# Kernel tuning notes

Measured on AMD Instinct MI355X. Metric: run time of the kernel, lower is better.

The kernel has to match this reference:

```python
import jax, jax.numpy as jnp
import numpy as np
import math

B, S, D, H = 2, 2048, 1024, 16
DH = D // H  # head_dim = 64


def setup_inputs() -> dict:
    key = jax.random.key(0)
    k0, k1, k2 = jax.random.split(key, 3)
    x = jax.random.normal(k0, (B, S, D), dtype=jnp.float32)
    Wi = jax.random.normal(k1, (3 * D, D), dtype=jnp.float32) * 0.02  # torch (out,in) layout
    bi = jnp.zeros((3 * D,), dtype=jnp.float32)
    Wo = jax.random.normal(k2, (D, D), dtype=jnp.float32) * 0.02
    bo = jnp.zeros((D,), dtype=jnp.float32)
    return {"x": x, "Wi": Wi, "bi": bi, "Wo": Wo, "bo": bo, "causal_mask": 1}


def reference(x, Wi, bi, Wo, bo, causal_mask):
    b, s, d = x.shape
    # fused QKV projection: nn.Linear applies x @ W.T + b
    qkv = x @ Wi.T + bi                      # (b, s, 3d)
    q, k, v = jnp.split(qkv, 3, axis=-1)
    # (b, s, d) -> (b, h, s, dh)
    def to_heads(t):
        return t.reshape(b, s, H, DH).transpose(0, 2, 1, 3)
    q, k, v = to_heads(q), to_heads(k), to_heads(v)
    scores = jnp.einsum("bhqd,bhkd->bhqk", q, k)  # (b, h, s, s)
    if causal_mask:
        # mask strictly-upper triangle with -inf BEFORE scaling (as in source; -inf unaffected)
        tri = jnp.triu(jnp.ones((s, s), dtype=bool), k=1)
        scores = jnp.where(tri, -jnp.inf, scores)
    scores = scores / math.sqrt(DH)
    weight = jax.nn.softmax(scores, axis=-1)
    out = jnp.einsum("bhqk,bhkd->bhqd", weight, v)  # (b, h, s, dh)
    out = out.transpose(0, 2, 1, 3).reshape(b, s, d)
    return out @ Wo.T + bo
```

## Files before the change

### kernel.cpp

```cpp
#include <hip/hip_runtime.h>
#include <hip/hip_bf16.h>
#include <stdint.h>

#define B_    2
#define S_    2048
#define D_    1024
#define H_    16
#define DH_   64
#define MTOT  (B_*S_)
#define NQKV  (3*D_)

typedef __attribute__((ext_vector_type(8))) short  bf16x8;
typedef __attribute__((ext_vector_type(4))) short  bf16x4;
typedef __attribute__((ext_vector_type(4))) float  f32x4;
typedef __attribute__((ext_vector_type(8))) unsigned short u16x8;
typedef unsigned short ushort_t;

__device__ __forceinline__ ushort_t f2bf(float f) {
  union { float f; unsigned int i; } v; v.f = f;
  unsigned int r = v.i + 0x7FFF + ((v.i >> 16) & 1);
  return (ushort_t)(r >> 16);
}

__device__ __forceinline__ unsigned cvt_pk_bf16(float lo, float hi) {
  unsigned r;
  asm("v_cvt_pk_bf16_f32 %0, %1, %2" : "=v"(r) : "v"(lo), "v"(hi));
  return r;
}

__device__ __forceinline__ float fexp2(float x) {
  float r;
  asm("v_exp_f32 %0, %1" : "=v"(r) : "v"(x));
  return r;
}

#if __has_builtin(__builtin_amdgcn_mfma_f32_16x16x16_bf16)
__device__ __forceinline__ f32x4 mfma16(bf16x4 a, bf16x4 b, f32x4 c) {
  return __builtin_amdgcn_mfma_f32_16x16x16_bf16(a, b, c, 0, 0, 0);
}
#elif __has_builtin(__builtin_amdgcn_mfma_f32_16x16x16bf16_1k)
__device__ __forceinline__ f32x4 mfma16(bf16x4 a, bf16x4 b, f32x4 c) {
  return __builtin_amdgcn_mfma_f32_16x16x16bf16_1k(a, b, c, 0, 0, 0);
}
#else
__device__ __forceinline__ f32x4 mfma16(bf16x4 a, bf16x4 b, f32x4 c) {
  asm volatile("v_mfma_f32_16x16x16_bf16 %0, %1, %2, %0"
               : "+v"(c) : "v"(a), "v"(b));
  return c;
}
#endif

__device__ __forceinline__ void gl_lds16(const ushort_t* g, ushort_t* l) {
  __builtin_amdgcn_global_load_lds(
      (const __attribute__((address_space(1))) unsigned int*)g,
      (__attribute__((address_space(3))) unsigned int*)l, 16, 0, 0);
}

#define CVN1 (MTOT*D_/8)
#define CVN2 (NQKV*D_/8)
#define CVN3 (D_*D_/8)
__global__ __launch_bounds__(256) void cvt_all(
    const float* __restrict__ x, const float* __restrict__ Wi, const float* __restrict__ Wo,
    ushort_t* __restrict__ xb, ushort_t* __restrict__ Wib, ushort_t* __restrict__ Wob) {
  int i = blockIdx.x * blockDim.x + threadIdx.x;
  const float* src; ushort_t* dst; int k;
  if (i < CVN1)            { src = x;  dst = xb;  k = i; }
  else if (i < CVN1+CVN2)  { src = Wi; dst = Wib; k = i - CVN1; }
  else                     { src = Wo; dst = Wob; k = i - CVN1 - CVN2; }
  const float4* s4 = (const float4*)src;
  float4 a = s4[2*k], b = s4[2*k+1];
  u16x8 o;
  o[0]=f2bf(a.x); o[1]=f2bf(a.y); o[2]=f2bf(a.z); o[3]=f2bf(a.w);
  o[4]=f2bf(b.x); o[5]=f2bf(b.y); o[6]=f2bf(b.z); o[7]=f2bf(b.w);
  ((u16x8*)dst)[k] = o;
}

#define BKg 32
#define QSCALE 0.18033688011112042f
__global__ __launch_bounds__(256) void gemm_qkv(
    const ushort_t* __restrict__ Abf, const ushort_t* __restrict__ Bbf,
    const float* __restrict__ bias,
    ushort_t* __restrict__ qb, ushort_t* __restrict__ kb, ushort_t* __restrict__ vb) {
  __shared__ __align__(16) ushort_t Al[128*BKg];
  __shared__ __align__(16) ushort_t Bl[128*BKg];
  int tid = threadIdx.x;
  int w = tid >> 6, lane = tid & 63;
  int wrow = (w >> 1) * 64, wcol = (w & 1) * 64;
  int m0 = blockIdx.y * 128, n0 = blockIdx.x * 128;
  const int K = D_;
  f32x4 zero = {0.f, 0.f, 0.f, 0.f};
  f32x4 acc[4][4];
  for (int i=0;i<4;i++) for (int j=0;j<4;j++) acc[i][j] = zero;

  for (int k0 = 0; k0 < K; k0 += BKg) {
    __syncthreads();
    for (int it = 0; it < 2; ++it) {
      int c = it*256 + tid;
      int row = c >> 2, cc = c & 3;
      int lbase = (it*256 + w*64) * 8;
      gl_lds16(Abf + (size_t)(m0+row)*K + k0 + cc*8, Al + lbase);
      gl_lds16(Bbf + (size_t)(n0+row)*K + k0 + cc*8, Bl + lbase);
    }
    asm volatile("s_waitcnt vmcnt(0)" ::: "memory");
    __syncthreads();
    int kof = (lane >> 4) * 8;
    bf16x8 af[4], bfr[4];
    for (int i=0;i<4;i++) af[i]  = *(const bf16x8*)(Al + (wrow + i*16 + (lane&15))*BKg + kof);
    for (int j=0;j<4;j++) bfr[j] = *(const bf16x8*)(Bl + (wcol + j*16 + (lane&15))*BKg + kof);
    for (int i=0;i<4;i++)
      for (int j=0;j<4;j++)
        acc[i][j] = __builtin_amdgcn_mfma_f32_16x16x32_bf16(af[i], bfr[j], acc[i][j], 0, 0, 0);
  }
  for (int i=0;i<4;i++)
    for (int j=0;j<4;j++)
      for (int r=0;r<4;r++) {
        int gm = m0 + wrow + i*16 + (lane>>4)*4 + r;
        int gn = n0 + wcol + j*16 + (lane&15);
        float v = acc[i][j][r] + bias[gn];
        int b = gm >> 11, s = gm & (S_-1);
        int sect = gn >> 10, hn = gn & (D_-1);
        int hh = hn >> 6, d = hn & 63;
        size_t idx = (((size_t)(b*H_ + hh))*S_ + s)*DH_ + d;
        if (sect == 0) v *= QSCALE;
        ushort_t val = f2bf(v);
        if (sect == 0) qb[idx] = val;
        else if (sect == 1) kb[idx] = val;
        else vb[idx] = val;
      }
}

__global__ __launch_bounds__(256) void transpose_v(
    const ushort_t* __restrict__ vb, ushort_t* __restrict__ vtb) {
  __shared__ ushort_t T[64*72];
  int bh = blockIdx.y;
  int s0 = blockIdx.x * 64;
  int tid = threadIdx.x;
  const ushort_t* src = vb + (size_t)bh * S_ * DH_;
  ushort_t* dst = vtb + (size_t)bh * DH_ * S_;
  for (int it = 0; it < 2; ++it) {
    int c = it*256 + tid;
    int row = c >> 3, cc = c & 7;
    *(uint4*)&T[row*72 + cc*8] = *(const uint4*)(src + (size_t)(s0+row)*DH_ + cc*8);
  }
  __syncthreads();
  for (int it = 0; it < 2; ++it) {
    int c = it*256 + tid;
    int d = c >> 3, sc = c & 7;
    u16x8 o;
    #pragma unroll
    for (int e = 0; e < 8; ++e) o[e] = T[(sc*8+e)*72 + d];
    *(u16x8*)(dst + (size_t)d*S_ + s0 + sc*8) = o;
  }
}

#define KVB 64
#define DTHR 8.0f
__global__ __launch_bounds__(512) void attn_fwd(
    const ushort_t* __restrict__ qb, const ushort_t* __restrict__ kb,
    const ushort_t* __restrict__ vtb, ushort_t* __restrict__ attnb,
    const int* __restrict__ causal) {
  int wg = blockIdx.x;
  int xcd = wg & 7;
  int rest = wg >> 3;
  int bh = (rest & 3) * 8 + xcd;
  int qblk = 15 - (rest >> 2);
  int b = bh >> 4, h = bh & 15;
  int tid = threadIdx.x, w = tid >> 6, lane = tid & 63;
  int g = lane >> 4, q16 = lane & 15;
  const ushort_t* qh  = qb  + (size_t)bh * S_ * DH_;
  const ushort_t* kh  = kb  + (size_t)bh * S_ * DH_;
  const ushort_t* vth = vtb + (size_t)bh * DH_ * S_;
  __shared__ __align__(16) ushort_t Kl[3][KVB*64];
  __shared__ __align__(16) ushort_t Vtl[3][64*KVB];
  bool use_causal = (causal[0] != 0);

  int nkv = use_causal ? (2*qblk + 2) : (S_/KVB);
  int qw = qblk*128 + w*16;

  bf16x8 qc0 = *(const bf16x8*)(qh + (size_t)(qw + q16)*DH_ +  0 + g*8);
  bf16x8 qc1 = *(const bf16x8*)(qh + (size_t)(qw + q16)*DH_ + 32 + g*8);

  int r0 = tid >> 3, sw0 = ((tid & 7) ^ (r0 & 7)) * 8;
  const ushort_t* kp0 = kh  + (size_t)r0 * DH_ + sw0;
  const ushort_t* vp0 = vth + (size_t)r0 * S_  + sw0;

  auto stage = [&](int t, int buf) {
    gl_lds16(kp0 + (size_t)(t*KVB) * DH_, &Kl[buf][tid*8]);
    gl_lds16(vp0 + t*KVB,                 &Vtl[buf][tid*8]);
  };

  f32x4 zero = {0.f,0.f,0.f,0.f};
  f32x4 o[4];
  #pragma unroll
  for (int dt=0;dt<4;dt++) o[dt] = zero;
  float mrun = -1e30f, lrun = 0.f;

  stage(0, 0);
  stage(1, 1);
  asm volatile("s_waitcnt vmcnt(2)" ::: "memory");
  __builtin_amdgcn_s_barrier();

  for (int it = 0; it < nkv; ++it) {
    int cur = it % 3;
    int kvbase = it * KVB;
    if (it + 2 < nkv) stage(it + 2, (it + 2) % 3);

    f32x4 sacc[4];
    #pragma unroll
    for (int j=0;j<4;j++) sacc[j] = zero;
    #pragma unroll
    for (int kk=0;kk<2;kk++) {
      bf16x8 qf = kk ? qc1 : qc0;
      #pragma unroll
      for (int j=0;j<4;j++) {
        int row = j*16 + q16;
        int slot = (kk*4 + g) ^ (row & 7);
        bf16x8 kf = *(const bf16x8*)(&Kl[cur][row*64 + slot*8]);
        sacc[j] = __builtin_amdgcn_mfma_f32_16x16x32_bf16(kf, qf, sacc[j], 0, 0, 0);
      }
    }
    if (use_causal && kvbase + KVB - 1 > qw) {
      int qd = qw + q16 - kvbase;
      #pragma unroll
      for (int j=0;j<4;j++)
        #pragma unroll
        for (int r=0;r<4;r++)
          if (16*j + 4*g + r > qd) sacc[j][r] = -1e30f;
    }
    float m0v = fmaxf(fmaxf(sacc[0][0], sacc[0][1]), fmaxf(sacc[0][2], sacc[0][3]));
    float m1v = fmaxf(fmaxf(sacc[1][0], sacc[1][1]), fmaxf(sacc[1][2], sacc[1][3]));
    float m2v = fmaxf(fmaxf(sacc[2][0], sacc[2][1]), fmaxf(sacc[2][2], sacc[2][3]));
    float m3v = fmaxf(fmaxf(sacc[3][0], sacc[3][1]), fmaxf(sacc[3][2], sacc[3][3]));
    float mx = fmaxf(fmaxf(m0v, m1v), fmaxf(m2v, m3v));
    mx = fmaxf(mx, __shfl_xor(mx, 16, 64));
    mx = fmaxf(mx, __shfl_xor(mx, 32, 64));
    if (!__all(mx - mrun <= DTHR)) {
      float mnew = fmaxf(mrun, mx);
      float alpha = fexp2(mrun - mnew);
      lrun *= alpha;
      float av0 = __shfl(alpha, 4*g + 0, 64);
      float av1 = __shfl(alpha, 4*g + 1, 64);
      float av2 = __shfl(alpha, 4*g + 2, 64);
      float av3 = __shfl(alpha, 4*g + 3, 64);
      #pragma unroll
      for (int dt=0;dt<4;dt++) {
        o[dt][0] *= av0; o[dt][1] *= av1; o[dt][2] *= av2; o[dt][3] *= av3;
      }
      mrun = mnew;
    }
    float p[4][4];
    float rs = 0.f;
    #pragma unroll
    for (int j=0;j<4;j++)
      #pragma unroll
      for (int r=0;r<4;r++) {
        p[j][r] = fexp2(sacc[j][r] - mrun);
        rs += p[j][r];
      }
    rs += __shfl_xor(rs, 16, 64);
    rs += __shfl_xor(rs, 32, 64);
    lrun += rs;
    #pragma unroll
    for (int s=0;s<4;s++) {
      union { unsigned u[2]; bf16x4 v; } pk;
      pk.u[0] = cvt_pk_bf16(p[s][0], p[s][1]);
      pk.u[1] = cvt_pk_bf16(p[s][2], p[s][3]);
      int E = 16*s + 4*g;
      #pragma unroll
      for (int dt=0;dt<4;dt++) {
        int row = dt*16 + q16;
        int off = row*64 + ((E >> 3) ^ (row & 7))*8 + (E & 7);
        bf16x4 vf = *(const bf16x4*)(&Vtl[cur][off]);
        o[dt] = mfma16(pk.v, vf, o[dt]);
      }
    }
    if (it + 2 < nkv) {
      asm volatile("s_waitcnt vmcnt(2)" ::: "memory");
    } else {
      asm volatile("s_waitcnt vmcnt(0)" ::: "memory");
    }
    __builtin_amdgcn_s_barrier();
  }
  float li0 = 1.f / __shfl(lrun, 4*g + 0, 64);
  float li1 = 1.f / __shfl(lrun, 4*g + 1, 64);
  float li2 = 1.f / __shfl(lrun, 4*g + 2, 64);
  float li3 = 1.f / __shfl(lrun, 4*g + 3, 64);
  #pragma unroll
  for (int r=0;r<4;r++) {
    float li = (r==0)?li0:(r==1)?li1:(r==2)?li2:li3;
    int q = qw + 4*g + r;
    #pragma unroll
    for (int dt=0;dt<4;dt++) {
      int d = dt*16 + q16;
      attnb[((size_t)(b*S_ + q))*D_ + h*DH_ + d] = f2bf(o[dt][r] * li);
    }
  }
}

__global__ __launch_bounds__(256) void gemm_out(
    const ushort_t* __restrict__ Abf, const ushort_t* __restrict__ Bbf,
    const float* __restrict__ bias, float* __restrict__ out) {
  __shared__ __align__(16) ushort_t Al[128*BKg];
  __shared__ __align__(16) ushort_t Bl[128*BKg];
  int tid = threadIdx.x;
  int w = tid >> 6, lane = tid & 63;
  int wrow = (w >> 1) * 64, wcol = (w & 1) * 64;
  int m0 = blockIdx.y * 128, n0 = blockIdx.x * 128;
  const int K = D_;
  f32x4 zero = {0.f,0.f,0.f,0.f};
  f32x4 acc[4][4];
  for (int i=0;i<4;i++) for (int j=0;j<4;j++) acc[i][j] = zero;

  for (int k0 = 0; k0 < K; k0 += BKg) {
    __syncthreads();
    for (int it = 0; it < 2; ++it) {
      int c = it*256 + tid;
      int row = c >> 2, cc = c & 3;
      int lbase = (it*256 + w*64) * 8;
      gl_lds16(Abf + (size_t)(m0+row)*K + k0 + cc*8, Al + lbase);
      gl_lds16(Bbf + (size_t)(n0+row)*K + k0 + cc*8, Bl + lbase);
    }
    asm volatile("s_waitcnt vmcnt(0)" ::: "memory");
    __syncthreads();
    int kof = (lane >> 4) * 8;
    bf16x8 af[4], bfr[4];
    for (int i=0;i<4;i++) af[i]  = *(const bf16x8*)(Al + (wrow + i*16 + (lane&15))*BKg + kof);
    for (int j=0;j<4;j++) bfr[j] = *(const bf16x8*)(Bl + (wcol + j*16 + (lane&15))*BKg + kof);
    for (int i=0;i<4;i++)
      for (int j=0;j<4;j++)
        acc[i][j] = __builtin_amdgcn_mfma_f32_16x16x32_bf16(af[i], bfr[j], acc[i][j], 0, 0, 0);
  }
  for (int i=0;i<4;i++)
    for (int j=0;j<4;j++)
      for (int r=0;r<4;r++) {
        int gm = m0 + wrow + i*16 + (lane>>4)*4 + r;
        int gn = n0 + wcol + j*16 + (lane&15);
        out[(size_t)gm*D_ + gn] = acc[i][j][r] + bias[gn];
      }
}

extern "C" void kernel_launch(void* const* d_in, const int* in_sizes, int n_in,
                              void* d_out, int out_size, void* d_ws, size_t ws_size,
                              hipStream_t stream) {
  const float* x  = (const float*)d_in[0];
  const float* Wi = (const float*)d_in[1];
  const float* bi = (const float*)d_in[2];
  const float* Wo = (const float*)d_in[3];
  const float* bo = (const float*)d_in[4];
  const int* causal = (const int*)d_in[5];
  float* out = (float*)d_out;

  ushort_t* xb   = (ushort_t*)d_ws;
  ushort_t* Wib  = xb  + (size_t)MTOT*D_;
  ushort_t* Wob  = Wib + (size_t)NQKV*D_;
  ushort_t* qbuf = Wob + (size_t)D_*D_;
  ushort_t* kbuf = qbuf + (size_t)B_*H_*S_*DH_;
  ushort_t* vbuf = kbuf + (size_t)B_*H_*S_*DH_;
  ushort_t* attnb = vbuf + (size_t)B_*H_*S_*DH_;
  ushort_t* vtb  = xb;

  int ntot = CVN1 + CVN2 + CVN3;
  cvt_all<<<(ntot+255)/256, 256, 0, stream>>>(x, Wi, Wo, xb, Wib, Wob);

  gemm_qkv<<<dim3(NQKV/128, MTOT/128), 256, 0, stream>>>(xb, Wib, bi, qbuf, kbuf, vbuf);
  transpose_v<<<dim3(S_/64, B_*H_), 256, 0, stream>>>(vbuf, vtb);
  attn_fwd<<<512, 512, 0, stream>>>(qbuf, kbuf, vtb, attnb, causal);
  gemm_out<<<dim3(D_/128, MTOT/128), 256, 0, stream>>>(attnb, Wob, bo, out);
}
```

Before: 123.3 us.

## Double-buffer GEMM LDS tiles and halve attention query block size

Both the QKV and output GEMMs now keep two LDS buffers. The next K-tile is prefetched while MFMAs run on the current one, which is meant to hide global-load latency that was previously serialized behind a full wait. The attention kernel moves from 128-query, 512-thread blocks to 64-query, 256-thread blocks, doubling the grid to 1024 workgroups for finer causal load balancing. Each thread now stages two K/V chunks. The cost is double the GEMM LDS footprint, plus more K/V reloads in attention because each block covers fewer queries.

```diff
diff --git a/kernel.cpp b/kernel.cpp
--- a/kernel.cpp
+++ b/kernel.cpp
@@ -81,35 +81,45 @@
     const ushort_t* __restrict__ Abf, const ushort_t* __restrict__ Bbf,
     const float* __restrict__ bias,
     ushort_t* __restrict__ qb, ushort_t* __restrict__ kb, ushort_t* __restrict__ vb) {
-  __shared__ __align__(16) ushort_t Al[128*BKg];
-  __shared__ __align__(16) ushort_t Bl[128*BKg];
+  __shared__ __align__(16) ushort_t Al[2][128*BKg];
+  __shared__ __align__(16) ushort_t Bl[2][128*BKg];
   int tid = threadIdx.x;
   int w = tid >> 6, lane = tid & 63;
   int wrow = (w >> 1) * 64, wcol = (w & 1) * 64;
   int m0 = blockIdx.y * 128, n0 = blockIdx.x * 128;
   const int K = D_;
-  f32x4 zero = {0.f, 0.f, 0.f, 0.f};
-  f32x4 acc[4][4];
-  for (int i=0;i<4;i++) for (int j=0;j<4;j++) acc[i][j] = zero;
-
-  for (int k0 = 0; k0 < K; k0 += BKg) {
-    __syncthreads();
+  const int nt = K / BKg;
+
+  auto stageg = [&](int t, int buf) {
+    int k0 = t * BKg;
+    #pragma unroll
     for (int it = 0; it < 2; ++it) {
       int c = it*256 + tid;
       int row = c >> 2, cc = c & 3;
       int lbase = (it*256 + w*64) * 8;
-      gl_lds16(Abf + (size_t)(m0+row)*K + k0 + cc*8, Al + lbase);
-      gl_lds16(Bbf + (size_t)(n0+row)*K + k0 + cc*8, Bl + lbase);
-    }
-    asm volatile("s_waitcnt vmcnt(0)" ::: "memory");
-    __syncthreads();
+      gl_lds16(Abf + (size_t)(m0+row)*K + k0 + cc*8, &Al[buf][lbase]);
+      gl_lds16(Bbf + (size_t)(n0+row)*K + k0 + cc*8, &Bl[buf][lbase]);
+    }
+  };
+
+  f32x4 zero = {0.f, 0.f, 0.f, 0.f};
+  f32x4 acc[4][4];
+  for (int i=0;i<4;i++) for (int j=0;j<4;j++) acc[i][j] = zero;
+
+  stageg(0, 0);
+  __syncthreads();
+
+  for (int t = 0; t < nt; ++t) {
+    int cur = t & 1;
+    if (t + 1 < nt) stageg(t + 1, cur ^ 1);
     int kof = (lane >> 4) * 8;
     bf16x8 af[4], bfr[4];
-    for (int i=0;i<4;i++) af[i]  = *(const bf16x8*)(Al + (wrow + i*16 + (lane&15))*BKg + kof);
-    for (int j=0;j<4;j++) bfr[j] = *(const bf16x8*)(Bl + (wcol + j*16 + (lane&15))*BKg + kof);
+    for (int i=0;i<4;i++) af[i]  = *(const bf16x8*)(&Al[cur][(wrow + i*16 + (lane&15))*BKg + kof]);
+    for (int j=0;j<4;j++) bfr[j] = *(const bf16x8*)(&Bl[cur][(wcol + j*16 + (lane&15))*BKg + kof]);
     for (int i=0;i<4;i++)
       for (int j=0;j<4;j++)
         acc[i][j] = __builtin_amdgcn_mfma_f32_16x16x32_bf16(af[i], bfr[j], acc[i][j], 0, 0, 0);
+    __syncthreads();
   }
   for (int i=0;i<4;i++)
     for (int j=0;j<4;j++)
@@ -155,7 +165,7 @@
 
 #define KVB 64
 #define DTHR 8.0f
-__global__ __launch_bounds__(512) void attn_fwd(
+__global__ __launch_bounds__(256) void attn_fwd(
     const ushort_t* __restrict__ qb, const ushort_t* __restrict__ kb,
     const ushort_t* __restrict__ vtb, ushort_t* __restrict__ attnb,
     const int* __restrict__ causal) {
@@ -163,7 +173,7 @@
   int xcd = wg & 7;
   int rest = wg >> 3;
   int bh = (rest & 3) * 8 + xcd;
-  int qblk = 15 - (rest >> 2);
+  int qblk = 31 - (rest >> 2);
   int b = bh >> 4, h = bh & 15;
   int tid = threadIdx.x, w = tid >> 6, lane = tid & 63;
   int g = lane >> 4, q16 = lane & 15;
@@ -174,19 +184,27 @@
   __shared__ __align__(16) ushort_t Vtl[3][64*KVB];
   bool use_causal = (causal[0] != 0);
 
-  int nkv = use_causal ? (2*qblk + 2) : (S_/KVB);
-  int qw = qblk*128 + w*16;
+  int nkv = use_causal ? (qblk + 1) : (S_/KVB);
+  int qw = qblk*64 + w*16;
 
   bf16x8 qc0 = *(const bf16x8*)(qh + (size_t)(qw + q16)*DH_ +  0 + g*8);
   bf16x8 qc1 = *(const bf16x8*)(qh + (size_t)(qw + q16)*DH_ + 32 + g*8);
 
-  int r0 = tid >> 3, sw0 = ((tid & 7) ^ (r0 & 7)) * 8;
-  const ushort_t* kp0 = kh  + (size_t)r0 * DH_ + sw0;
-  const ushort_t* vp0 = vth + (size_t)r0 * S_  + sw0;
+  int c0 = tid, c1 = tid + 256;
+  int r0 = c0 >> 3, sw0 = ((c0 & 7) ^ (r0 & 7)) * 8;
+  int r1 = c1 >> 3, sw1 = ((c1 & 7) ^ (r1 & 7)) * 8;
+  const ushort_t* kp0 = kh + r0*DH_ + sw0;
+  const ushort_t* kp1 = kh + r1*DH_ + sw1;
+  const ushort_t* vp0 = vth + (size_t)r0*S_ + sw0;
+  const ushort_t* vp1 = vth + (size_t)r1*S_ + sw1;
 
   auto stage = [&](int t, int buf) {
-    gl_lds16(kp0 + (size_t)(t*KVB) * DH_, &Kl[buf][tid*8]);
-    gl_lds16(vp0 + t*KVB,                 &Vtl[buf][tid*8]);
+    size_t kadv = (size_t)(t*KVB) * DH_;
+    int vadv = t*KVB;
+    gl_lds16(kp0 + kadv, &Kl[buf][c0*8]);
+    gl_lds16(kp1 + kadv, &Kl[buf][c1*8]);
+    gl_lds16(vp0 + vadv, &Vtl[buf][c0*8]);
+    gl_lds16(vp1 + vadv, &Vtl[buf][c1*8]);
   };
 
   f32x4 zero = {0.f,0.f,0.f,0.f};
@@ -197,7 +215,7 @@
 
   stage(0, 0);
   stage(1, 1);
-  asm volatile("s_waitcnt vmcnt(2)" ::: "memory");
+  asm volatile("s_waitcnt vmcnt(4)" ::: "memory");
   __builtin_amdgcn_s_barrier();
 
   for (int it = 0; it < nkv; ++it) {
@@ -275,7 +293,7 @@
       }
     }
     if (it + 2 < nkv) {
-      asm volatile("s_waitcnt vmcnt(2)" ::: "memory");
+      asm volatile("s_waitcnt vmcnt(4)" ::: "memory");
     } else {
       asm volatile("s_waitcnt vmcnt(0)" ::: "memory");
     }
@@ -300,35 +318,45 @@
 __global__ __launch_bounds__(256) void gemm_out(
     const ushort_t* __restrict__ Abf, const ushort_t* __restrict__ Bbf,
     const float* __restrict__ bias, float* __restrict__ out) {
-  __shared__ __align__(16) ushort_t Al[128*BKg];
-  __shared__ __align__(16) ushort_t Bl[128*BKg];
+  __shared__ __align__(16) ushort_t Al[2][128*BKg];
+  __shared__ __align__(16) ushort_t Bl[2][128*BKg];
   int tid = threadIdx.x;
   int w = tid >> 6, lane = tid & 63;
   int wrow = (w >> 1) * 64, wcol = (w & 1) * 64;
   int m0 = blockIdx.y * 128, n0 = blockIdx.x * 128;
   const int K = D_;
-  f32x4 zero = {0.f,0.f,0.f,0.f};
-  f32x4 acc[4][4];
-  for (int i=0;i<4;i++) for (int j=0;j<4;j++) acc[i][j] = zero;
-
-  for (int k0 = 0; k0 < K; k0 += BKg) {
-    __syncthreads();
+  const int nt = K / BKg;
+
+  auto stageg = [&](int t, int buf) {
+    int k0 = t * BKg;
+    #pragma unroll
     for (int it = 0; it < 2; ++it) {
       int c = it*256 + tid;
       int row = c >> 2, cc = c & 3;
       int lbase = (it*256 + w*64) * 8;
-      gl_lds16(Abf + (size_t)(m0+row)*K + k0 + cc*8, Al + lbase);
-      gl_lds16(Bbf + (size_t)(n0+row)*K + k0 + cc*8, Bl + lbase);
-    }
-    asm volatile("s_waitcnt vmcnt(0)" ::: "memory");
-    __syncthreads();
+      gl_lds16(Abf + (size_t)(m0+row)*K + k0 + cc*8, &Al[buf][lbase]);
+      gl_lds16(Bbf + (size_t)(n0+row)*K + k0 + cc*8, &Bl[buf][lbase]);
+    }
+  };
+
+  f32x4 zero = {0.f,0.f,0.f,0.f};
+  f32x4 acc[4][4];
+  for (int i=0;i<4;i++) for (int j=0;j<4;j++) acc[i][j] = zero;
+
+  stageg(0, 0);
+  __syncthreads();
+
+  for (int t = 0; t < nt; ++t) {
+    int cur = t & 1;
+    if (t + 1 < nt) stageg(t + 1, cur ^ 1);
     int kof = (lane >> 4) * 8;
     bf16x8 af[4], bfr[4];
-    for (int i=0;i<4;i++) af[i]  = *(const bf16x8*)(Al + (wrow + i*16 + (lane&15))*BKg + kof);
-    for (int j=0;j<4;j++) bfr[j] = *(const bf16x8*)(Bl + (wcol + j*16 + (lane&15))*BKg + kof);
+    for (int i=0;i<4;i++) af[i]  = *(const bf16x8*)(&Al[cur][(wrow + i*16 + (lane&15))*BKg + kof]);
+    for (int j=0;j<4;j++) bfr[j] = *(const bf16x8*)(&Bl[cur][(wcol + j*16 + (lane&15))*BKg + kof]);
     for (int i=0;i<4;i++)
       for (int j=0;j<4;j++)
         acc[i][j] = __builtin_amdgcn_mfma_f32_16x16x32_bf16(af[i], bfr[j], acc[i][j], 0, 0, 0);
+    __syncthreads();
   }
   for (int i=0;i<4;i++)
     for (int j=0;j<4;j++)
@@ -364,6 +392,6 @@
 
   gemm_qkv<<<dim3(NQKV/128, MTOT/128), 256, 0, stream>>>(xb, Wib, bi, qbuf, kbuf, vbuf);
   transpose_v<<<dim3(S_/64, B_*H_), 256, 0, stream>>>(vbuf, vtb);
-  attn_fwd<<<512, 512, 0, stream>>>(qbuf, kbuf, vtb, attnb, causal);
+  attn_fwd<<<1024, 256, 0, stream>>>(qbuf, kbuf, vtb, attnb, causal);
   gemm_out<<<dim3(D_/128, MTOT/128), 256, 0, stream>>>(attnb, Wob, bo, out);
 }
```

Measured after the change: 130.9 us. 1.06x slower.

## Use persistent attention blocks with per-XCD atomic work queues and smaller query tiles

Applied to the files above, without the earlier changes.

Turns attention into a persistent kernel of 768 blocks of 256 threads. Each block pulls work items from eight per-XCD atomic counters, longest causal rows first, and can steal from other queues once its own is empty. Query tiles shrink from 128 to 64 rows, and the counters are reset inside the conversion kernel. The goal is better load balance across the triangular causal workload; the cost is atomics, extra barriers and less K/V reuse per staged tile.

```diff
diff --git a/kernel.cpp b/kernel.cpp
--- a/kernel.cpp
+++ b/kernel.cpp
@@ -61,8 +61,10 @@
 #define CVN3 (D_*D_/8)
 __global__ __launch_bounds__(256) void cvt_all(
     const float* __restrict__ x, const float* __restrict__ Wi, const float* __restrict__ Wo,
-    ushort_t* __restrict__ xb, ushort_t* __restrict__ Wib, ushort_t* __restrict__ Wob) {
+    ushort_t* __restrict__ xb, ushort_t* __restrict__ Wib, ushort_t* __restrict__ Wob,
+    int* __restrict__ ctr) {
   int i = blockIdx.x * blockDim.x + threadIdx.x;
+  if (i < 8) ctr[i] = 0;
   const float* src; ushort_t* dst; int k;
   if (i < CVN1)            { src = x;  dst = xb;  k = i; }
   else if (i < CVN1+CVN2)  { src = Wi; dst = Wib; k = i - CVN1; }
@@ -155,144 +157,162 @@
 
 #define KVB 64
 #define DTHR 8.0f
-__global__ __launch_bounds__(512) void attn_fwd(
+__global__ __launch_bounds__(256) void attn_fwd(
     const ushort_t* __restrict__ qb, const ushort_t* __restrict__ kb,
     const ushort_t* __restrict__ vtb, ushort_t* __restrict__ attnb,
-    const int* __restrict__ causal) {
-  int wg = blockIdx.x;
-  int xcd = wg & 7;
-  int rest = wg >> 3;
-  int bh = (rest & 3) * 8 + xcd;
-  int qblk = 15 - (rest >> 2);
-  int b = bh >> 4, h = bh & 15;
+    const int* __restrict__ causal, int* __restrict__ ctr) {
   int tid = threadIdx.x, w = tid >> 6, lane = tid & 63;
   int g = lane >> 4, q16 = lane & 15;
-  const ushort_t* qh  = qb  + (size_t)bh * S_ * DH_;
-  const ushort_t* kh  = kb  + (size_t)bh * S_ * DH_;
-  const ushort_t* vth = vtb + (size_t)bh * DH_ * S_;
   __shared__ __align__(16) ushort_t Kl[3][KVB*64];
   __shared__ __align__(16) ushort_t Vtl[3][64*KVB];
+  __shared__ int e_sh;
   bool use_causal = (causal[0] != 0);
-
-  int nkv = use_causal ? (2*qblk + 2) : (S_/KVB);
-  int qw = qblk*128 + w*16;
-
-  bf16x8 qc0 = *(const bf16x8*)(qh + (size_t)(qw + q16)*DH_ +  0 + g*8);
-  bf16x8 qc1 = *(const bf16x8*)(qh + (size_t)(qw + q16)*DH_ + 32 + g*8);
-
-  int r0 = tid >> 3, sw0 = ((tid & 7) ^ (r0 & 7)) * 8;
-  const ushort_t* kp0 = kh  + (size_t)r0 * DH_ + sw0;
-  const ushort_t* vp0 = vth + (size_t)r0 * S_  + sw0;
-
-  auto stage = [&](int t, int buf) {
-    gl_lds16(kp0 + (size_t)(t*KVB) * DH_, &Kl[buf][tid*8]);
-    gl_lds16(vp0 + t*KVB,                 &Vtl[buf][tid*8]);
-  };
+  int myq = blockIdx.x & 7;
 
   f32x4 zero = {0.f,0.f,0.f,0.f};
-  f32x4 o[4];
-  #pragma unroll
-  for (int dt=0;dt<4;dt++) o[dt] = zero;
-  float mrun = -1e30f, lrun = 0.f;
-
-  stage(0, 0);
-  stage(1, 1);
-  asm volatile("s_waitcnt vmcnt(2)" ::: "memory");
-  __builtin_amdgcn_s_barrier();
-
-  for (int it = 0; it < nkv; ++it) {
-    int cur = it % 3;
-    int kvbase = it * KVB;
-    if (it + 2 < nkv) stage(it + 2, (it + 2) % 3);
-
-    f32x4 sacc[4];
-    #pragma unroll
-    for (int j=0;j<4;j++) sacc[j] = zero;
-    #pragma unroll
-    for (int kk=0;kk<2;kk++) {
-      bf16x8 qf = kk ? qc1 : qc0;
+
+  for (int qi = 0; qi < 8; ++qi) {
+    int qq = (myq + qi) & 7;
+    while (true) {
+      if (tid == 0) e_sh = atomicAdd(&ctr[qq], 1);
+      __syncthreads();
+      int e = e_sh;
+      if (e >= 128) break;
+      int qblk = 31 - (e >> 2);
+      int bh = qq + 8 * (e & 3);
+      int b = bh >> 4, h = bh & 15;
+      const ushort_t* qh  = qb  + (size_t)bh * S_ * DH_;
+      const ushort_t* kh  = kb  + (size_t)bh * S_ * DH_;
+      const ushort_t* vth = vtb + (size_t)bh * DH_ * S_;
+
+      int nkv = use_causal ? (qblk + 1) : (S_/KVB);
+      int qw = qblk*64 + w*16;
+
+      bf16x8 qc0 = *(const bf16x8*)(qh + (size_t)(qw + q16)*DH_ +  0 + g*8);
+      bf16x8 qc1 = *(const bf16x8*)(qh + (size_t)(qw + q16)*DH_ + 32 + g*8);
+
+      int c0 = tid, c1 = tid + 256;
+      int r0 = c0 >> 3, sw0 = ((c0 & 7) ^ (r0 & 7)) * 8;
+      int r1 = c1 >> 3, sw1 = ((c1 & 7) ^ (r1 & 7)) * 8;
+      const ushort_t* kp0 = kh + r0*DH_ + sw0;
+      const ushort_t* kp1 = kh + r1*DH_ + sw1;
+      const ushort_t* vp0 = vth + (size_t)r0*S_ + sw0;
+      const ushort_t* vp1 = vth + (size_t)r1*S_ + sw1;
+
+      auto stage = [&](int t, int buf) {
+        size_t kadv = (size_t)(t*KVB) * DH_;
+        int vadv = t*KVB;
+        gl_lds16(kp0 + kadv, &Kl[buf][c0*8]);
+        gl_lds16(kp1 + kadv, &Kl[buf][c1*8]);
+        gl_lds16(vp0 + vadv, &Vtl[buf][c0*8]);
+        gl_lds16(vp1 + vadv, &Vtl[buf][c1*8]);
+      };
+
+      f32x4 o[4];
       #pragma unroll
-      for (int j=0;j<4;j++) {
-        int row = j*16 + q16;
-        int slot = (kk*4 + g) ^ (row & 7);
-        bf16x8 kf = *(const bf16x8*)(&Kl[cur][row*64 + slot*8]);
-        sacc[j] = __builtin_amdgcn_mfma_f32_16x16x32_bf16(kf, qf, sacc[j], 0, 0, 0);
+      for (int dt=0;dt<4;dt++) o[dt] = zero;
+      float mrun = -1e30f, lrun = 0.f;
+
+      stage(0, 0);
+      stage(1, 1);
+      asm volatile("s_waitcnt vmcnt(4)" ::: "memory");
+      __builtin_amdgcn_s_barrier();
+
+      for (int it = 0; it < nkv; ++it) {
+        int cur = it % 3;
+        int kvbase = it * KVB;
+        if (it + 2 < nkv) stage(it + 2, (it + 2) % 3);
+
+        f32x4 sacc[4];
+        #pragma unroll
+        for (int j=0;j<4;j++) sacc[j] = zero;
+        #pragma unroll
+        for (int kk=0;kk<2;kk++) {
+          bf16x8 qf = kk ? qc1 : qc0;
+          #pragma unroll
+          for (int j=0;j<4;j++) {
+            int row = j*16 + q16;
+            int slot = (kk*4 + g) ^ (row & 7);
+            bf16x8 kf = *(const bf16x8*)(&Kl[cur][row*64 + slot*8]);
+            sacc[j] = __builtin_amdgcn_mfma_f32_16x16x32_bf16(kf, qf, sacc[j], 0, 0, 0);
+          }
+        }
+        if (use_causal && kvbase + KVB - 1 > qw) {
+          int qd = qw + q16 - kvbase;
+          #pragma unroll
+          for (int j=0;j<4;j++)
+            #pragma unroll
+            for (int r=0;r<4;r++)
+              if (16*j + 4*g + r > qd) sacc[j][r] = -1e30f;
+        }
+        float m0v = fmaxf(fmaxf(sacc[0][0], sacc[0][1]), fmaxf(sacc[0][2], sacc[0][3]));
+        float m1v = fmaxf(fmaxf(sacc[1][0], sacc[1][1]), fmaxf(sacc[1][2], sacc[1][3]));
+        float m2v = fmaxf(fmaxf(sacc[2][0], sacc[2][1]), fmaxf(sacc[2][2], sacc[2][3]));
+        float m3v = fmaxf(fmaxf(sacc[3][0], sacc[3][1]), fmaxf(sacc[3][2], sacc[3][3]));
+        float mx = fmaxf(fmaxf(m0v, m1v), fmaxf(m2v, m3v));
+        mx = fmaxf(mx, __shfl_xor(mx, 16, 64));
+        mx = fmaxf(mx, __shfl_xor(mx, 32, 64));
+        if (!__all(mx - mrun <= DTHR)) {
+          float mnew = fmaxf(mrun, mx);
+          float alpha = fexp2(mrun - mnew);
+          lrun *= alpha;
+          float av0 = __shfl(alpha, 4*g + 0, 64);
+          float av1 = __shfl(alpha, 4*g + 1, 64);
+          float av2 = __shfl(alpha, 4*g + 2, 64);
+          float av3 = __shfl(alpha, 4*g + 3, 64);
+          #pragma unroll
+          for (int dt=0;dt<4;dt++) {
+            o[dt][0] *= av0; o[dt][1] *= av1; o[dt][2] *= av2; o[dt][3] *= av3;
+          }
+          mrun = mnew;
+        }
+        float p[4][4];
+        float rs = 0.f;
+        #pragma unroll
+        for (int j=0;j<4;j++)
+          #pragma unroll
+          for (int r=0;r<4;r++) {
+            p[j][r] = fexp2(sacc[j][r] - mrun);
+            rs += p[j][r];
+          }
+        rs += __shfl_xor(rs, 16, 64);
+        rs += __shfl_xor(rs, 32, 64);
+        lrun += rs;
+        #pragma unroll
+        for (int s=0;s<4;s++) {
+          union { unsigned u[2]; bf16x4 v; } pk;
+          pk.u[0] = cvt_pk_bf16(p[s][0], p[s][1]);
+          pk.u[1] = cvt_pk_bf16(p[s][2], p[s][3]);
+          int E = 16*s + 4*g;
+          #pragma unroll
+          for (int dt=0;dt<4;dt++) {
+            int row = dt*16 + q16;
+            int off = row*64 + ((E >> 3) ^ (row & 7))*8 + (E & 7);
+            bf16x4 vf = *(const bf16x4*)(&Vtl[cur][off]);
+            o[dt] = mfma16(pk.v, vf, o[dt]);
+          }
+        }
+        if (it + 2 < nkv) {
+          asm volatile("s_waitcnt vmcnt(4)" ::: "memory");
+        } else {
+          asm volatile("s_waitcnt vmcnt(0)" ::: "memory");
+        }
+        __builtin_amdgcn_s_barrier();
       }
-    }
-    if (use_causal && kvbase + KVB - 1 > qw) {
-      int qd = qw + q16 - kvbase;
-      #pragma unroll
-      for (int j=0;j<4;j++)
-        #pragma unroll
-        for (int r=0;r<4;r++)
-          if (16*j + 4*g + r > qd) sacc[j][r] = -1e30f;
-    }
-    float m0v = fmaxf(fmaxf(sacc[0][0], sacc[0][1]), fmaxf(sacc[0][2], sacc[0][3]));
-    float m1v = fmaxf(fmaxf(sacc[1][0], sacc[1][1]), fmaxf(sacc[1][2], sacc[1][3]));
-    float m2v = fmaxf(fmaxf(sacc[2][0], sacc[2][1]), fmaxf(sacc[2][2], sacc[2][3]));
-    float m3v = fmaxf(fmaxf(sacc[3][0], sacc[3][1]), fmaxf(sacc[3][2], sacc[3][3]));
-    float mx = fmaxf(fmaxf(m0v, m1v), fmaxf(m2v, m3v));
-    mx = fmaxf(mx, __shfl_xor(mx, 16, 64));
-    mx = fmaxf(mx, __shfl_xor(mx, 32, 64));
-    if (!__all(mx - mrun <= DTHR)) {
-      float mnew = fmaxf(mrun, mx);
-      float alpha = fexp2(mrun - mnew);
-      lrun *= alpha;
-      float av0 = __shfl(alpha, 4*g + 0, 64);
-      float av1 = __shfl(alpha, 4*g + 1, 64);
-      float av2 = __shfl(alpha, 4*g + 2, 64);
-      float av3 = __shfl(alpha, 4*g + 3, 64);
-      #pragma unroll
-      for (int dt=0;dt<4;dt++) {
-        o[dt][0] *= av0; o[dt][1] *= av1; o[dt][2] *= av2; o[dt][3] *= av3;
-      }
-      mrun = mnew;
-    }
-    float p[4][4];
-    float rs = 0.f;
-    #pragma unroll
-    for (int j=0;j<4;j++)
+      float li0 = 1.f / __shfl(lrun, 4*g + 0, 64);
+      float li1 = 1.f / __shfl(lrun, 4*g + 1, 64);
+      float li2 = 1.f / __shfl(lrun, 4*g + 2, 64);
+      float li3 = 1.f / __shfl(lrun, 4*g + 3, 64);
       #pragma unroll
       for (int r=0;r<4;r++) {
-        p[j][r] = fexp2(sacc[j][r] - mrun);
-        rs += p[j][r];
+        float li = (r==0)?li0:(r==1)?li1:(r==2)?li2:li3;
+        int q = qw + 4*g + r;
+        #pragma unroll
+        for (int dt=0;dt<4;dt++) {
+          int d = dt*16 + q16;
+          attnb[((size_t)(b*S_ + q))*D_ + h*DH_ + d] = f2bf(o[dt][r] * li);
+        }
       }
-    rs += __shfl_xor(rs, 16, 64);
-    rs += __shfl_xor(rs, 32, 64);
-    lrun += rs;
-    #pragma unroll
-    for (int s=0;s<4;s++) {
-      union { unsigned u[2]; bf16x4 v; } pk;
-      pk.u[0] = cvt_pk_bf16(p[s][0], p[s][1]);
-      pk.u[1] = cvt_pk_bf16(p[s][2], p[s][3]);
-      int E = 16*s + 4*g;
-      #pragma unroll
-      for (int dt=0;dt<4;dt++) {
-        int row = dt*16 + q16;
-        int off = row*64 + ((E >> 3) ^ (row & 7))*8 + (E & 7);
-        bf16x4 vf = *(const bf16x4*)(&Vtl[cur][off]);
-        o[dt] = mfma16(pk.v, vf, o[dt]);
-      }
-    }
-    if (it + 2 < nkv) {
-      asm volatile("s_waitcnt vmcnt(2)" ::: "memory");
-    } else {
-      asm volatile("s_waitcnt vmcnt(0)" ::: "memory");
-    }
-    __builtin_amdgcn_s_barrier();
-  }
-  float li0 = 1.f / __shfl(lrun, 4*g + 0, 64);
-  float li1 = 1.f / __shfl(lrun, 4*g + 1, 64);
-  float li2 = 1.f / __shfl(lrun, 4*g + 2, 64);
-  float li3 = 1.f / __shfl(lrun, 4*g + 3, 64);
-  #pragma unroll
-  for (int r=0;r<4;r++) {
-    float li = (r==0)?li0:(r==1)?li1:(r==2)?li2:li3;
-    int q = qw + 4*g + r;
-    #pragma unroll
-    for (int dt=0;dt<4;dt++) {
-      int d = dt*16 + q16;
-      attnb[((size_t)(b*S_ + q))*D_ + h*DH_ + d] = f2bf(o[dt][r] * li);
     }
   }
 }
@@ -357,13 +377,14 @@
   ushort_t* kbuf = qbuf + (size_t)B_*H_*S_*DH_;
   ushort_t* vbuf = kbuf + (size_t)B_*H_*S_*DH_;
   ushort_t* attnb = vbuf + (size_t)B_*H_*S_*DH_;
+  int* ctr = (int*)(attnb + (size_t)MTOT*D_);
   ushort_t* vtb  = xb;
 
   int ntot = CVN1 + CVN2 + CVN3;
-  cvt_all<<<(ntot+255)/256, 256, 0, stream>>>(x, Wi, Wo, xb, Wib, Wob);
+  cvt_all<<<(ntot+255)/256, 256, 0, stream>>>(x, Wi, Wo, xb, Wib, Wob, ctr);
 
   gemm_qkv<<<dim3(NQKV/128, MTOT/128), 256, 0, stream>>>(xb, Wib, bi, qbuf, kbuf, vbuf);
   transpose_v<<<dim3(S_/64, B_*H_), 256, 0, stream>>>(vbuf, vtb);
-  attn_fwd<<<512, 512, 0, stream>>>(qbuf, kbuf, vtb, attnb, causal);
+  attn_fwd<<<768, 256, 0, stream>>>(qbuf, kbuf, vtb, attnb, causal, ctr);
   gemm_out<<<dim3(D_/128, MTOT/128), 256, 0, stream>>>(attnb, Wob, bo, out);
 }
```

Measured after the change: 184.3 us. 49.6% more time.
